# Kernel tuning notes

Measured on AMD Instinct MI355X. Metric: run time of the kernel, lower is better.

## Reference

```python
import jax, jax.numpy as jnp
import numpy as np

HEADS = 16

def setup_inputs() -> dict:
    key = jax.random.key(0)
    k1, k2, k3 = jax.random.split(key, 3)
    b, t, d = 2, 2048, 1024
    x = jax.random.normal(k1, (b, t, d), dtype=jnp.float32)
    w_qkv = jax.random.normal(k2, (d, 3 * d), dtype=jnp.float32) * (d ** -0.5)
    w_out = jax.random.normal(k3, (d, d), dtype=jnp.float32) * (d ** -0.5)
    b_out = jnp.zeros((d,), dtype=jnp.float32)
    return {"x": x, "w_qkv": w_qkv, "w_out": w_out, "b_out": b_out}

def reference(x, w_qkv, w_out, b_out):
    b, t, d = x.shape
    h = HEADS
    dh = d // h
    qkv = x @ w_qkv                      # [b, t, 3d]
    q, k, v = jnp.split(qkv, 3, axis=-1)
    split_heads = lambda a: a.reshape(b, t, h, dh).transpose(0, 2, 1, 3)  # [b,h,t,dh]
    q, k, v = map(split_heads, (q, k, v))
    # NOTE: faithful to source — no 1/sqrt(dh) scaling, causal=False so no mask
    dots = jnp.einsum('bhid,bhjd->bhij', q, k)      # [b,h,t,t]
    attn = jax.nn.softmax(dots, axis=-1)
    out = jnp.einsum('bhjd,bhij->bhid', v, attn)    # [b,h,t,dh]
    out = out.transpose(0, 2, 1, 3).reshape(b, t, d)
    return out @ w_out + b_out
```

## Files before the change

### kernel.cpp

```cpp
#include <hip/hip_runtime.h>
#include <hip/hip_bf16.h>
#include <stdint.h>

typedef __attribute__((ext_vector_type(4))) float f32x4;
typedef __attribute__((ext_vector_type(8))) short bf16x8;

#define MFMA(a, b, c) __builtin_amdgcn_mfma_f32_16x16x32_bf16((a), (b), (c), 0, 0, 0)
#define BAR do { __builtin_amdgcn_s_barrier(); asm volatile("" ::: "memory"); } while (0)

template <int N> __device__ __forceinline__ void waitcnt_vm() {
  if constexpr (N == 0) asm volatile("s_waitcnt vmcnt(0)" ::: "memory");
  else if constexpr (N == 3) asm volatile("s_waitcnt vmcnt(3)" ::: "memory");
  else if constexpr (N == 4) asm volatile("s_waitcnt vmcnt(4)" ::: "memory");
}

__device__ __forceinline__ uint16_t f2b(float f) {
  uint32_t u = __builtin_bit_cast(uint32_t, f);
  uint32_t r = (u + 0x7FFFu + ((u >> 16) & 1u)) >> 16;
  return (uint16_t)r;
}

__device__ __forceinline__ uint32_t cvt_pk_bf16(float lo, float hi) {
  uint32_t r;
  asm("v_cvt_pk_bf16_f32 %0, %1, %2" : "=v"(r) : "v"(lo), "v"(hi));
  return r;
}

__device__ __forceinline__ float fexp2(float x) {
  float r;
  asm("v_exp_f32 %0, %1" : "=v"(r) : "v"(x));
  return r;
}

__device__ __forceinline__ void dot2_acc(float& l, uint32_t p, uint32_t ones2) {
  asm("v_dot2_f32_bf16 %0, %1, %2, %0" : "+v"(l) : "v"(p), "v"(ones2));
}

__device__ __forceinline__ void gld_lds16(const void* g, void* l) {
  __builtin_amdgcn_global_load_lds((const __attribute__((address_space(1))) uint32_t*)g,
                                   (__attribute__((address_space(3))) uint32_t*)l, 16, 0, 0);
}

__device__ __forceinline__ int swz(int r) {
  return (r & 3) | ((((r >> 2) ^ (r >> 3)) & 1) << 2);
}

__global__ __launch_bounds__(256) void prologue(const float* __restrict__ x,
                                                const float* __restrict__ wqkv,
                                                const float* __restrict__ wout,
                                                uint16_t* __restrict__ xb,
                                                uint16_t* __restrict__ wqkvT,
                                                uint16_t* __restrict__ woutT) {
  __shared__ float t_[32][33];
  const int bid = blockIdx.x;
  if (bid < 4096) {
    const int i = (bid * 256 + threadIdx.x) * 4;
    const float4 v = *(const float4*)(x + i);
    ushort4 o;
    o.x = f2b(v.x); o.y = f2b(v.y); o.z = f2b(v.z); o.w = f2b(v.w);
    *(ushort4*)(xb + i) = o;
    return;
  }
  const float* in;
  uint16_t* out;
  int C, bx, by;
  if (bid < 7168) { in = wqkv; out = wqkvT; C = 3072; bx = (bid - 4096) % 96; by = (bid - 4096) / 96; }
  else            { in = wout; out = woutT; C = 1024; bx = (bid - 7168) & 31;  by = (bid - 7168) >> 5; }
  const int R = 1024;
  const int c0 = bx * 32, r0 = by * 32;
  const int tx = threadIdx.x & 31, ty = threadIdx.x >> 5;
#pragma unroll
  for (int i = 0; i < 4; i++)
    t_[ty + i * 8][tx] = in[(size_t)(r0 + ty + i * 8) * C + c0 + tx];
  __syncthreads();
#pragma unroll
  for (int i = 0; i < 4; i++)
    out[(size_t)(c0 + ty + i * 8) * R + r0 + tx] = f2b(t_[tx][ty + i * 8]);
}

template <int NOUT, int BN, bool BF16_OUT, bool BIAS, bool SCALEQ, bool VSPLIT>
__global__ __launch_bounds__(256) void gemm_bt(const uint16_t* __restrict__ A,
                                               const uint16_t* __restrict__ Bt,
                                               const float* __restrict__ bias,
                                               void* __restrict__ Cout,
                                               uint16_t* __restrict__ VTout) {
  constexpr int NF = BN / 32;
  constexpr int TILEB = 8192 + BN * 64;
  constexpr int NL = 2 + BN / 64;
  __shared__ __align__(16) char LDS[3 * TILEB];
  const int tid = threadIdx.x;
  const int wave = tid >> 6, lane = tid & 63;
  const int lr = lane & 15, lg = lane >> 4;

  const int nwg = gridDim.x * gridDim.y;
  const int id0 = blockIdx.y * gridDim.x + blockIdx.x;
  const int sid = (id0 & 7) * (nwg >> 3) + (id0 >> 3);
  const int row0 = (sid / gridDim.x) * 128, col0 = (sid % gridDim.x) * BN;
  const int wr = (wave >> 1) * 64, wc = (wave & 1) * (BN / 2);

  f32x4 acc[4][NF] = {};

  const int ldsOff = wave * 1024 + lane * 16;
  const int srow = ldsOff >> 6, scolB = ldsOff & 63;
  const char* ApA = (const char*)A + ((size_t)(row0 + srow) * 1024) * 2 + scolB;
  const char* ApB = ApA + 64 * 2048;
  const char* BpA = (const char*)Bt + ((size_t)(col0 + srow) * 1024) * 2 + scolB;
  const char* BpB = BpA + 64 * 2048;

  auto stage = [&](int t, char* base) {
    char* d = base + wave * 1024;
    const int kk = t * 64;
    gld_lds16(ApA + kk, d);
    gld_lds16(ApB + kk, d + 4096);
    gld_lds16(BpA + kk, d + 8192);
    if constexpr (BN == 128) gld_lds16(BpB + kk, d + 12288);
  };
  auto compute = [&](const char* S) {
    bf16x8 af[4], bfv[NF];
#pragma unroll
    for (int i = 0; i < 4; i++)
      af[i] = *(const bf16x8*)(S + (wr + i * 16 + lr) * 64 + lg * 16);
#pragma unroll
    for (int j = 0; j < NF; j++)
      bfv[j] = *(const bf16x8*)(S + 8192 + (wc + j * 16 + lr) * 64 + lg * 16);
    __builtin_amdgcn_s_setprio(1);
#pragma unroll
    for (int i = 0; i < 4; i++)
#pragma unroll
      for (int j = 0; j < NF; j++)
        acc[i][j] = MFMA(af[i], bfv[j], acc[i][j]);
    __builtin_amdgcn_s_setprio(0);
  };

  stage(0, LDS);
  stage(1, LDS + TILEB);
#pragma unroll 1
  for (int i = 0; i < 30; i += 3) {
    waitcnt_vm<NL>(); BAR; stage(i + 2, LDS + 2 * TILEB); compute(LDS);
    waitcnt_vm<NL>(); BAR; stage(i + 3, LDS);             compute(LDS + TILEB);
    waitcnt_vm<NL>(); BAR; stage(i + 4, LDS + TILEB);     compute(LDS + 2 * TILEB);
  }
  waitcnt_vm<NL>(); BAR; compute(LDS);
  waitcnt_vm<0>();  BAR; compute(LDS + TILEB);

  const float qs = (SCALEQ && col0 < 1024) ? 1.4426950408889634f : 1.0f;
#pragma unroll
  for (int i = 0; i < 4; i++)
#pragma unroll
    for (int j = 0; j < NF; j++) {
      const int col = col0 + wc + j * 16 + lr;
      const int rowb = row0 + wr + i * 16 + lg * 4;
      if (VSPLIT && col >= 2048) {
        ushort4 vs;
        vs.x = f2b(acc[i][j][0]); vs.y = f2b(acc[i][j][1]);
        vs.z = f2b(acc[i][j][2]); vs.w = f2b(acc[i][j][3]);
        const int bIdx = rowb >> 11, tok = rowb & 2047;
        *(ushort4*)(VTout + (size_t)(bIdx * 1024 + (col - 2048)) * 2048 + tok) = vs;
      } else {
        const float bv = BIAS ? bias[col] : 0.f;
#pragma unroll
        for (int r = 0; r < 4; r++) {
          const float v = acc[i][j][r] * qs + bv;
          if (BF16_OUT) ((uint16_t*)Cout)[(size_t)(rowb + r) * NOUT + col] = f2b(v);
          else          ((float*)Cout)[(size_t)(rowb + r) * NOUT + col] = v;
        }
      }
    }
}

__global__ __launch_bounds__(256) void attn_fwd(const uint16_t* __restrict__ qkv,
                                                const uint16_t* __restrict__ VT,
                                                uint16_t* __restrict__ O) {
  __shared__ __align__(16) char LDS[3 * 16384];
  const int tid = threadIdx.x;
  const int wave = tid >> 6, lane = tid & 63;
  const int lr = lane & 15, lg = lane >> 4;
  const int id = blockIdx.x;
  const int w = id >> 3;
  const int bh = (id & 7) * 4 + (w >> 4);
  const int qt = w & 15;
  const int b = bh >> 4, h = bh & 15;
  const int q0 = qt * 128 + wave * 32;

  const uint16_t* Qp = qkv + (size_t)(b * 2048 + q0 + lr) * 3072 + h * 64 + lg * 8;
  const bf16x8 qA0 = *(const bf16x8*)Qp;
  const bf16x8 qA1 = *(const bf16x8*)(Qp + 32);
  const bf16x8 qB0 = *(const bf16x8*)(Qp + 16 * 3072);
  const bf16x8 qB1 = *(const bf16x8*)(Qp + 16 * 3072 + 32);

  const int off1 = wave * 1024 + lane * 16;
  const int off2 = off1 + 4096;
  const int r1 = off1 >> 7, c1 = (off1 >> 4) & 7;
  const int r2 = off2 >> 7, c2 = (off2 >> 4) & 7;
  const char* qb = (const char*)qkv;
  const char* vb = (const char*)VT;
  const char* Kp1 = qb + ((size_t)(b * 2048 + r1) * 3072 + 1024 + h * 64) * 2 + (c1 ^ swz(r1)) * 16;
  const char* Kp2 = qb + ((size_t)(b * 2048 + r2) * 3072 + 1024 + h * 64) * 2 + (c2 ^ swz(r2)) * 16;
  const char* Vp1 = vb + ((size_t)(bh * 64 + r1) * 2048) * 2 + (c1 ^ swz(r1)) * 16;
  const char* Vp2 = vb + ((size_t)(bh * 64 + r2) * 2048) * 2 + (c2 ^ swz(r2)) * 16;

  const int wb1 = wave * 1024;
  const int wb2 = 4096 + wave * 1024;

  auto stage = [&](size_t t, char* slot) {
    const size_t ka = t * 393216;
    const int va = (int)t * 128;
    gld_lds16(Kp1 + ka, slot + wb1);
    gld_lds16(Kp2 + ka, slot + wb2);
    gld_lds16(Vp1 + va, slot + 8192 + wb1);
    gld_lds16(Vp2 + va, slot + 8192 + wb2);
  };

  int koff[8], voff[8];
  const int rbase = ((lr >> 2) << 3) | (lr & 3);
#pragma unroll
  for (int fj = 0; fj < 4; fj++) {
    const int row = rbase + ((fj & 1) << 2) + ((fj >> 1) << 5);
    const int sw = swz(row);
    koff[fj * 2]     = row * 128 + ((lg ^ sw) * 16);
    koff[fj * 2 + 1] = row * 128 + (((4 + lg) ^ sw) * 16);
  }
#pragma unroll
  for (int cf = 0; cf < 4; cf++) {
    const int dr = cf * 16 + lr;
    const int sw = swz(dr);
    voff[cf * 2]     = 8192 + dr * 128 + ((lg ^ sw) * 16);
    voff[cf * 2 + 1] = 8192 + dr * 128 + (((4 + lg) ^ sw) * 16);
  }

  f32x4 oA[4] = {}, oB[4] = {};
  float lA0 = 0.f, lA1 = 0.f, lB0 = 0.f, lB1 = 0.f;
  const uint32_t ones2 = 0x3F803F80u;
  const f32x4 z4 = {0.f, 0.f, 0.f, 0.f};
  const char* ldsB = (const char*)LDS;

  union PW { uint32_t u[8]; struct { bf16x8 a0, a1; } f; };

  auto compute = [&](int sb) {
    f32x4 s0[4], s1[4];
    __builtin_amdgcn_s_setprio(1);
#pragma unroll
    for (int fj = 0; fj < 4; fj++) {
      const bf16x8 k0 = *(const bf16x8*)(ldsB + sb + koff[fj * 2]);
      const bf16x8 k1 = *(const bf16x8*)(ldsB + sb + koff[fj * 2 + 1]);
      s0[fj] = MFMA(k0, qA0, z4);
      s0[fj] = MFMA(k1, qA1, s0[fj]);
      s1[fj] = MFMA(k0, qB0, z4);
      s1[fj] = MFMA(k1, qB1, s1[fj]);
    }
    __builtin_amdgcn_s_setprio(0);
    bf16x8 v0[4], v1[4];
#pragma unroll
    for (int cf = 0; cf < 4; cf++) {
      v0[cf] = *(const bf16x8*)(ldsB + sb + voff[cf * 2]);
      v1[cf] = *(const bf16x8*)(ldsB + sb + voff[cf * 2 + 1]);
    }
    PW pA, pB;
#pragma unroll
    for (int fj = 0; fj < 4; fj++) {
      const float a0 = fexp2(s0[fj][0]), a1 = fexp2(s0[fj][1]);
      const float a2 = fexp2(s0[fj][2]), a3 = fexp2(s0[fj][3]);
      pA.u[fj * 2]     = cvt_pk_bf16(a0, a1);
      pA.u[fj * 2 + 1] = cvt_pk_bf16(a2, a3);
      const float b0 = fexp2(s1[fj][0]), b1 = fexp2(s1[fj][1]);
      const float b2 = fexp2(s1[fj][2]), b3 = fexp2(s1[fj][3]);
      pB.u[fj * 2]     = cvt_pk_bf16(b0, b1);
      pB.u[fj * 2 + 1] = cvt_pk_bf16(b2, b3);
    }
#pragma unroll
    for (int j = 0; j < 8; j += 2) {
      dot2_acc(lA0, pA.u[j], ones2);
      dot2_acc(lA1, pA.u[j + 1], ones2);
      dot2_acc(lB0, pB.u[j], ones2);
      dot2_acc(lB1, pB.u[j + 1], ones2);
    }
    __builtin_amdgcn_s_setprio(1);
#pragma unroll
    for (int cf = 0; cf < 4; cf++) {
      oA[cf] = MFMA(pA.f.a0, v0[cf], oA[cf]);
      oA[cf] = MFMA(pA.f.a1, v1[cf], oA[cf]);
      oB[cf] = MFMA(pB.f.a0, v0[cf], oB[cf]);
      oB[cf] = MFMA(pB.f.a1, v1[cf], oB[cf]);
    }
    __builtin_amdgcn_s_setprio(0);
  };

  stage(0, LDS);
  stage(1, LDS + 16384);
#pragma unroll 1
  for (int t = 0; t < 30; t += 3) {
    waitcnt_vm<4>(); BAR; stage(t + 2, LDS + 32768); compute(0);
    waitcnt_vm<4>(); BAR; stage(t + 3, LDS);         compute(16384);
    waitcnt_vm<4>(); BAR; stage(t + 4, LDS + 16384); compute(32768);
  }
  waitcnt_vm<4>(); BAR; compute(0);
  waitcnt_vm<0>(); BAR; compute(16384);

  float lA = lA0 + lA1, lB = lB0 + lB1;
  lA += __shfl_xor(lA, 16, 64); lA += __shfl_xor(lA, 32, 64);
  lB += __shfl_xor(lB, 16, 64); lB += __shfl_xor(lB, 32, 64);

  float invA[4], invB[4];
#pragma unroll
  for (int r = 0; r < 4; r++) {
    invA[r] = 1.0f / __shfl(lA, lg * 4 + r, 64);
    invB[r] = 1.0f / __shfl(lB, lg * 4 + r, 64);
  }
#pragma unroll
  for (int cf = 0; cf < 4; cf++)
#pragma unroll
    for (int r = 0; r < 4; r++) {
      const int col = h * 64 + cf * 16 + lr;
      const int rowA = b * 2048 + q0 + lg * 4 + r;
      O[(size_t)rowA * 1024 + col] = f2b(oA[cf][r] * invA[r]);
      O[(size_t)(rowA + 16) * 1024 + col] = f2b(oB[cf][r] * invB[r]);
    }
}

extern "C" void kernel_launch(void* const* d_in, const int* in_sizes, int n_in,
                              void* d_out, int out_size, void* d_ws, size_t ws_size,
                              hipStream_t stream) {
  const float* x    = (const float*)d_in[0];
  const float* wqkv = (const float*)d_in[1];
  const float* wout = (const float*)d_in[2];
  const float* bout = (const float*)d_in[3];

  char* ws = (char*)d_ws;
  uint16_t* woutT   = (uint16_t*)(ws + 0);
  uint16_t* qkvb    = (uint16_t*)(ws + (2ull  << 20));
  uint16_t* VT      = (uint16_t*)(ws + (26ull << 20));
  uint16_t* xb      = (uint16_t*)(ws + (34ull << 20));
  uint16_t* wqkvT   = (uint16_t*)(ws + (42ull << 20));
  uint16_t* attnout = xb;

  prologue<<<dim3(8192), dim3(256), 0, stream>>>(x, wqkv, wout, xb, wqkvT, woutT);

  gemm_bt<3072, 128, true, false, true, true>
      <<<dim3(24, 32), dim3(256), 0, stream>>>(xb, wqkvT, nullptr, qkvb, VT);
  attn_fwd<<<dim3(512), dim3(256), 0, stream>>>(qkvb, VT, attnout);
  gemm_bt<1024, 64, false, true, false, false>
      <<<dim3(16, 32), dim3(256), 0, stream>>>(attnout, woutT, bout, d_out, nullptr);
}
```

Before: 105.4 us.

## Shrink attention blocks to two waves with double-buffered K/V staging

The attention kernel now runs 1024 blocks of 128 threads, each covering 64 queries, instead of 512 blocks of 256 threads. The K/V pipeline drops from triple to double buffering, which cuts LDS per block from 48KB to 32KB and lets more blocks share a CU. Each thread now issues four loads per tensor per stage, and each step adds an extra barrier. Each block loads the full K/V for its head, so K/V global and L2 traffic doubles and there is less prefetch distance to hide latency.

```diff
diff --git a/kernel.cpp b/kernel.cpp
--- a/kernel.cpp
+++ b/kernel.cpp
@@ -12,6 +12,7 @@
   if constexpr (N == 0) asm volatile("s_waitcnt vmcnt(0)" ::: "memory");
   else if constexpr (N == 3) asm volatile("s_waitcnt vmcnt(3)" ::: "memory");
   else if constexpr (N == 4) asm volatile("s_waitcnt vmcnt(4)" ::: "memory");
+  else if constexpr (N == 8) asm volatile("s_waitcnt vmcnt(8)" ::: "memory");
 }
 
 __device__ __forceinline__ uint16_t f2b(float f) {
@@ -168,19 +169,19 @@
     }
 }
 
-__global__ __launch_bounds__(256) void attn_fwd(const uint16_t* __restrict__ qkv,
+__global__ __launch_bounds__(128) void attn_fwd(const uint16_t* __restrict__ qkv,
                                                 const uint16_t* __restrict__ VT,
                                                 uint16_t* __restrict__ O) {
-  __shared__ __align__(16) char LDS[3 * 16384];
+  __shared__ __align__(16) char LDS[2 * 16384];
   const int tid = threadIdx.x;
   const int wave = tid >> 6, lane = tid & 63;
   const int lr = lane & 15, lg = lane >> 4;
   const int id = blockIdx.x;
   const int w = id >> 3;
-  const int bh = (id & 7) * 4 + (w >> 4);
-  const int qt = w & 15;
+  const int bh = (id & 7) * 4 + (w >> 5);
+  const int qt = w & 31;
   const int b = bh >> 4, h = bh & 15;
-  const int q0 = qt * 128 + wave * 32;
+  const int q0 = qt * 64 + wave * 32;
 
   const uint16_t* Qp = qkv + (size_t)(b * 2048 + q0 + lr) * 3072 + h * 64 + lg * 8;
   const bf16x8 qA0 = *(const bf16x8*)Qp;
@@ -188,27 +189,28 @@
   const bf16x8 qB0 = *(const bf16x8*)(Qp + 16 * 3072);
   const bf16x8 qB1 = *(const bf16x8*)(Qp + 16 * 3072 + 32);
 
-  const int off1 = wave * 1024 + lane * 16;
-  const int off2 = off1 + 4096;
-  const int r1 = off1 >> 7, c1 = (off1 >> 4) & 7;
-  const int r2 = off2 >> 7, c2 = (off2 >> 4) & 7;
   const char* qb = (const char*)qkv;
   const char* vb = (const char*)VT;
-  const char* Kp1 = qb + ((size_t)(b * 2048 + r1) * 3072 + 1024 + h * 64) * 2 + (c1 ^ swz(r1)) * 16;
-  const char* Kp2 = qb + ((size_t)(b * 2048 + r2) * 3072 + 1024 + h * 64) * 2 + (c2 ^ swz(r2)) * 16;
-  const char* Vp1 = vb + ((size_t)(bh * 64 + r1) * 2048) * 2 + (c1 ^ swz(r1)) * 16;
-  const char* Vp2 = vb + ((size_t)(bh * 64 + r2) * 2048) * 2 + (c2 ^ swz(r2)) * 16;
-
-  const int wb1 = wave * 1024;
-  const int wb2 = 4096 + wave * 1024;
+  const char* Kp[4];
+  const char* Vp[4];
+#pragma unroll
+  for (int i = 0; i < 4; i++) {
+    const int c = tid + 128 * i;
+    const int row = c >> 3, col = c & 7;
+    const int scol = col ^ swz(row);
+    Kp[i] = qb + ((size_t)(b * 2048 + row) * 3072 + 1024 + h * 64) * 2 + scol * 16;
+    Vp[i] = vb + ((size_t)(bh * 64 + row) * 2048) * 2 + scol * 16;
+  }
+  const int wb = wave * 1024;
 
   auto stage = [&](size_t t, char* slot) {
     const size_t ka = t * 393216;
     const int va = (int)t * 128;
-    gld_lds16(Kp1 + ka, slot + wb1);
-    gld_lds16(Kp2 + ka, slot + wb2);
-    gld_lds16(Vp1 + va, slot + 8192 + wb1);
-    gld_lds16(Vp2 + va, slot + 8192 + wb2);
+#pragma unroll
+    for (int i = 0; i < 4; i++) {
+      gld_lds16(Kp[i] + ka, slot + wb + i * 2048);
+      gld_lds16(Vp[i] + va, slot + 8192 + wb + i * 2048);
+    }
   };
 
   int koff[8], voff[8];
@@ -286,14 +288,19 @@
   };
 
   stage(0, LDS);
-  stage(1, LDS + 16384);
 #pragma unroll 1
-  for (int t = 0; t < 30; t += 3) {
-    waitcnt_vm<4>(); BAR; stage(t + 2, LDS + 32768); compute(0);
-    waitcnt_vm<4>(); BAR; stage(t + 3, LDS);         compute(16384);
-    waitcnt_vm<4>(); BAR; stage(t + 4, LDS + 16384); compute(32768);
-  }
-  waitcnt_vm<4>(); BAR; compute(0);
+  for (int t = 0; t < 30; t += 2) {
+    BAR;
+    stage(t + 1, LDS + 16384);
+    waitcnt_vm<8>(); BAR;
+    compute(0);
+    BAR;
+    stage(t + 2, LDS);
+    waitcnt_vm<8>(); BAR;
+    compute(16384);
+  }
+  BAR; stage(31, LDS + 16384);
+  waitcnt_vm<8>(); BAR; compute(0);
   waitcnt_vm<0>(); BAR; compute(16384);
 
   float lA = lA0 + lA1, lB = lB0 + lB1;
@@ -337,7 +344,7 @@
 
   gemm_bt<3072, 128, true, false, true, true>
       <<<dim3(24, 32), dim3(256), 0, stream>>>(xb, wqkvT, nullptr, qkvb, VT);
-  attn_fwd<<<dim3(512), dim3(256), 0, stream>>>(qkvb, VT, attnout);
+  attn_fwd<<<dim3(1024), dim3(128), 0, stream>>>(qkvb, VT, attnout);
   gemm_bt<1024, 64, false, true, false, false>
       <<<dim3(16, 32), dim3(256), 0, stream>>>(attnout, woutT, bout, d_out, nullptr);
 }
```

After: 110.2 us. +4.6%, slower.
